# Performance work log

Hardware: AMD Instinct MI355X
Metric: run time of the kernel (lower is better)

## Reference

```python
import jax, jax.numpy as jnp
import numpy as np
import math

D_QKV = 64


def setup_inputs() -> dict:
    key = jax.random.key(0)
    ks = jax.random.split(key, 6)
    b, l, d_model, n_head, d_qkv = 2, 2048, 1024, 16, D_QKV
    return {
        "x": jax.random.normal(ks[0], (b, l, d_model), dtype=jnp.float32),
        "w_q": jax.random.normal(ks[1], (n_head, d_model, d_qkv), dtype=jnp.float32) * (2.0 / (d_model + d_qkv)) ** 0.5,
        "w_k": jax.random.normal(ks[2], (n_head, d_model, d_qkv), dtype=jnp.float32) * (2.0 / (d_model + d_qkv)) ** 0.5,
        "w_v": jax.random.normal(ks[3], (n_head, d_model, d_qkv), dtype=jnp.float32) * (2.0 / (d_model + d_qkv)) ** 0.5,
        "w_o": jax.random.normal(ks[4], (n_head, d_qkv, d_model), dtype=jnp.float32) * (2.0 / (d_model + d_qkv)) ** 0.5,
        "mask": jnp.zeros((b, 1, 1, l), dtype=bool),  # True = masked (padding)
    }


def reference(x, w_q, w_k, w_v, w_o, mask):
    # x: [b, l, m]; w_{q,k,v}: [n, m, d]; w_o: [n, d, m]; mask broadcastable to [b, n, l, l]
    q = jnp.einsum("blm,nmd->bnld", x, w_q)
    k = jnp.einsum("blm,nmd->bnld", x, w_k)
    v = jnp.einsum("blm,nmd->bnld", x, w_v)
    scores = jnp.einsum("bnld,bnkd->bnlk", q, k) / math.sqrt(D_QKV)
    scores = jnp.where(mask, jnp.float32(-1e9), scores)
    attn = jax.nn.softmax(scores, axis=-1)  # dropout is identity (p=0 / eval)
    ctx = jnp.einsum("bnlk,bnkd->bnld", attn, v)
    # per-head output projection then sum over heads: V.matmul(w_o).sum(dim=1)
    return jnp.einsum("bnld,ndm->blm", ctx, w_o)
```

## Files before the change

### kernel.cpp

```cpp
#include <hip/hip_runtime.h>
#include <stdint.h>

using bf16x8  = __attribute__((ext_vector_type(8))) short;
using f32x4   = __attribute__((ext_vector_type(4))) float;
using f32x16  = __attribute__((ext_vector_type(16))) float;
using ushort8 = __attribute__((ext_vector_type(8))) unsigned short;
using ushort4v= __attribute__((ext_vector_type(4))) unsigned short;
using uint2v  = __attribute__((ext_vector_type(2))) unsigned int;

typedef __attribute__((address_space(1))) const unsigned int* gas_ptr;
typedef __attribute__((address_space(3))) unsigned int*       las_ptr;

__device__ __forceinline__ void gload_lds16(const unsigned short* g, unsigned short* l) {
    __builtin_amdgcn_global_load_lds((gas_ptr)(const void*)g, (las_ptr)(void*)l, 16, 0, 0);
}

__device__ __forceinline__ unsigned short f2bf(float f) {
    union { float f; uint32_t u; } x; x.f = f;
    uint32_t u = x.u;
    uint32_t r = u + 0x7fffu + ((u >> 16) & 1u);
    return (unsigned short)(r >> 16);
}
__device__ __forceinline__ float bf2f(unsigned short u) {
    union { uint32_t u; float f; } x; x.u = ((uint32_t)u) << 16;
    return x.f;
}

__device__ __forceinline__ f32x4 mfma16(bf16x8 a, bf16x8 b, f32x4 c) {
    return __builtin_amdgcn_mfma_f32_16x16x32_bf16(a, b, c, 0, 0, 0);
}
__device__ __forceinline__ f32x16 mfma32(bf16x8 a, bf16x8 b, f32x16 c) {
    return __builtin_amdgcn_mfma_f32_32x32x16_bf16(a, b, c, 0, 0, 0);
}

__device__ __forceinline__ unsigned int cvtpk_bf16(float lo, float hi) {
    unsigned int r;
    asm("v_cvt_pk_bf16_f32 %0, %1, %2" : "=v"(r) : "v"(lo), "v"(hi));
    return r;
}
__device__ __forceinline__ void plswap(unsigned int& a, unsigned int& b) {
    asm("v_permlane32_swap_b32 %0, %1" : "+v"(a), "+v"(b));
}


__global__ void cast_x_kernel(const float* __restrict__ x, unsigned short* __restrict__ xb) {
    int i = blockIdx.x * 256 + threadIdx.x;
    using f32x4v = __attribute__((ext_vector_type(4))) float;
    f32x4v v = ((const f32x4v*)x)[i];
    ushort4v o;
    o[0] = f2bf(v[0]); o[1] = f2bf(v[1]); o[2] = f2bf(v[2]); o[3] = f2bf(v[3]);
    ((ushort4v*)xb)[i] = o;
}

__global__ void pack_wqkv_t(const float* __restrict__ wq, const float* __restrict__ wk,
                            const float* __restrict__ wv, unsigned short* __restrict__ wpT) {
    __shared__ float tile[64][65];
    const int mm = blockIdx.y;
    const int s = mm >> 4, hh = mm & 15;
    const float* src = ((s == 0) ? wq : (s == 1) ? wk : wv) + (size_t)hh * 1024 * 64;
    const int k0 = blockIdx.x * 64;
    const int c = threadIdx.x & 63, rg = threadIdx.x >> 6;
#pragma unroll
    for (int i = 0; i < 16; ++i) {
        int r = rg * 16 + i;
        tile[r][c] = src[(size_t)(k0 + r) * 64 + c];
    }
    __syncthreads();
    unsigned short* dst = wpT + ((size_t)s * 1024 + hh * 64) * 1024 + k0;
    const int kc = threadIdx.x & 63, dg = threadIdx.x >> 6;
#pragma unroll
    for (int i = 0; i < 16; ++i) {
        int d = dg * 16 + i;
        dst[(size_t)d * 1024 + kc] = f2bf(tile[kc][d]);
    }
}

__global__ void pack_wo_t(const float* __restrict__ wo, unsigned short* __restrict__ woT) {
    __shared__ float tile[64][65];
    const int r0 = blockIdx.y * 64;
    const int c0 = blockIdx.x * 64;
    const int c = threadIdx.x & 63, rg = threadIdx.x >> 6;
#pragma unroll
    for (int i = 0; i < 16; ++i) {
        int r = rg * 16 + i;
        tile[r][c] = wo[(size_t)(r0 + r) * 1024 + c0 + c];
    }
    __syncthreads();
    const int kc = threadIdx.x & 63, mg = threadIdx.x >> 6;
#pragma unroll
    for (int i = 0; i < 16; ++i) {
        int m = mg * 16 + i;
        woT[(size_t)(c0 + m) * 1024 + r0 + kc] = f2bf(tile[kc][m]);
    }
}

__global__ void vt_kernel(const unsigned short* __restrict__ vb, unsigned short* __restrict__ vtb) {
    __shared__ unsigned short tile[64][72];
    const int bh = blockIdx.y;
    const int l0 = blockIdx.x * 64;
    const unsigned short* src = vb + (size_t)bh * 131072;
    unsigned short* dst = vtb + (size_t)bh * 131072;
    const int c8 = threadIdx.x & 7, r2 = threadIdx.x >> 3;
#pragma unroll
    for (int it = 0; it < 2; ++it) {
        int r = r2 + it * 32;
        ushort8 v = *(const ushort8*)&src[(size_t)(l0 + r) * 64 + c8 * 8];
        *(ushort8*)&tile[r][c8 * 8] = v;
    }
    __syncthreads();
#pragma unroll
    for (int it = 0; it < 2; ++it) {
        int d = r2 + it * 32;
        ushort8 o;
#pragma unroll
        for (int j = 0; j < 8; ++j) o[j] = tile[c8 * 8 + j][d];
        *(ushort8*)&dst[(size_t)d * 2048 + l0 + c8 * 8] = o;
    }
}


template<int MODE, int BN>
__global__ __launch_bounds__(256) void gemm_bt(
    const unsigned short* __restrict__ A,
    const unsigned short* __restrict__ BT,
    float* __restrict__ Cf,
    unsigned short* __restrict__ Q,
    unsigned short* __restrict__ Kq,
    unsigned short* __restrict__ V,
    int M, int N, int K)
{
    constexpr int NF = BN / 32;
    __shared__ unsigned short As[128 * 64];
    __shared__ unsigned short Bs[BN * 64];
    const int tid  = threadIdx.x;
    const int lane = tid & 63;
    const int wave = tid >> 6;
    const int wm = wave >> 1, wn = wave & 1;
    const int l15 = lane & 15, l4 = lane >> 4;
    const int row0 = blockIdx.y * 128;
    const int col0 = blockIdx.x * BN;

    f32x4 acc[4][NF];
#pragma unroll
    for (int i = 0; i < 4; ++i)
#pragma unroll
        for (int j = 0; j < NF; ++j) acc[i][j] = (f32x4){0.f, 0.f, 0.f, 0.f};

    for (int k0 = 0; k0 < K; k0 += 64) {
        __syncthreads();
#pragma unroll
        for (int it = 0; it < 4; ++it) {
            int cb = (it * 4 + wave) * 64;
            int c  = cb + lane;
            int r  = c >> 3, c8 = c & 7;
            int sc8 = c8 ^ (r & 7);
            gload_lds16(&A[(size_t)(row0 + r) * K + k0 + sc8 * 8], &As[cb * 8]);
        }
#pragma unroll
        for (int it = 0; it < NF; ++it) {
            int cb = (it * 4 + wave) * 64;
            int c  = cb + lane;
            int r  = c >> 3, c8 = c & 7;
            int sc8 = c8 ^ (r & 7);
            gload_lds16(&BT[(size_t)(col0 + r) * K + k0 + sc8 * 8], &Bs[cb * 8]);
        }
        __syncthreads();
#pragma unroll
        for (int kk = 0; kk < 2; ++kk) {
            bf16x8 af[4], bfr[NF];
#pragma unroll
            for (int m = 0; m < 4; ++m) {
                int r   = wm * 64 + m * 16 + l15;
                int blk = (kk * 4 + l4) ^ (r & 7);
                af[m] = *(const bf16x8*)&As[r * 64 + blk * 8];
            }
#pragma unroll
            for (int n = 0; n < NF; ++n) {
                int r   = wn * (BN / 2) + n * 16 + l15;
                int blk = (kk * 4 + l4) ^ (r & 7);
                bfr[n] = *(const bf16x8*)&Bs[r * 64 + blk * 8];
            }
#pragma unroll
            for (int m = 0; m < 4; ++m)
#pragma unroll
                for (int n = 0; n < NF; ++n)
                    acc[m][n] = mfma16(af[m], bfr[n], acc[m][n]);
        }
    }

#pragma unroll
    for (int m = 0; m < 4; ++m) {
#pragma unroll
        for (int n = 0; n < NF; ++n) {
#pragma unroll
            for (int r = 0; r < 4; ++r) {
                int gr = row0 + wm * 64 + m * 16 + l4 * 4 + r;
                int gc = col0 + wn * (BN / 2) + n * 16 + l15;
                float v = acc[m][n][r];
                if (MODE == 0) {
                    int s = gc >> 10, rem = gc & 1023;
                    int hh = rem >> 6, dd = rem & 63;
                    int bb = gr >> 11, ll = gr & 2047;
                    unsigned short* dst = (s == 0) ? Q : (s == 1) ? Kq : V;
                    dst[(((size_t)bb * 16 + hh) * 2048 + ll) * 64 + dd] = f2bf(v);
                } else {
                    Cf[(size_t)gr * N + gc] = v;
                }
            }
        }
    }
}


__global__ __launch_bounds__(256, 4) void attn_kernel(
    const unsigned short* __restrict__ qb,
    const unsigned short* __restrict__ kb,
    const unsigned short* __restrict__ vtb,
    const unsigned char* __restrict__ mask,
    unsigned short* __restrict__ part0,
    unsigned short* __restrict__ part1,
    float* __restrict__ ml)
{
    const int lg = blockIdx.x;
    int u = ((lg & 7) << 7) | (lg >> 3);
    int bh = u >> 5, sub = u & 31;
    const int qt = sub >> 1, half = sub & 1;
    const int b = bh >> 4, h = bh & 15;
    const int t0 = half * 16;
    const int NT = 16;

    const int tid  = threadIdx.x;
    const int lane = tid & 63, wave = tid >> 6;
    const int l31  = lane & 31, hi = lane >> 5;

    __shared__ unsigned short smem[16384];
    __shared__ int flags[32];

    const size_t hoff = (size_t)bh * 131072;
    const unsigned short* qh  = qb  + hoff;
    const unsigned short* kh  = kb  + hoff;
    const unsigned short* vth = vtb + hoff;
    const unsigned char*  mb  = mask + (size_t)b * 2048;

    if (tid < 32) flags[tid] = 0;
    __syncthreads();
    {
        uint2v mv = *(const uint2v*)&mb[tid * 8];
        if (mv[0] | mv[1]) flags[tid >> 3] = 1;
    }

    const int qrow = qt * 128 + wave * 32 + l31;
    bf16x8 qf[4];
#pragma unroll
    for (int ki = 0; ki < 4; ++ki)
        qf[ki] = *(const bf16x8*)&qh[(size_t)qrow * 64 + ki * 16 + hi * 8];

    f32x16 accA = {0,0,0,0,0,0,0,0,0,0,0,0,0,0,0,0};
    f32x16 accB = {0,0,0,0,0,0,0,0,0,0,0,0,0,0,0,0};
    float m_r = -1e30f, l_r = 0.f;
    const float SC  = 0.18033688011112042f;
    const float THR = 44.3614195558365f;

#define STAGE(KB, VB, KV0) do {                                                          \
        _Pragma("unroll")                                                                \
        for (int it_ = 0; it_ < 2; ++it_) {                                              \
            int c_ = it_ * 256 + tid;                                                    \
            int r_ = c_ >> 3, c8_ = c_ & 7;                                              \
            int sc8_ = c8_ ^ (r_ & 7);                                                   \
            gload_lds16(&kh[(size_t)((KV0) + r_) * 64 + sc8_ * 8],                       \
                        &(KB)[(it_ * 256 + wave * 64) * 8]);                             \
            gload_lds16(&vth[(size_t)r_ * 2048 + (KV0) + sc8_ * 8],                      \
                        &(VB)[(it_ * 256 + wave * 64) * 8]);                             \
        }                                                                                \
    } while (0)

    STAGE(smem, smem + 8192, t0 * 64);

    for (int t = t0; t < t0 + NT; ++t) {
        const int kv0 = t * 64;
        unsigned short* Kb = smem + ((t - t0) & 1) * 4096;
        unsigned short* Vb = smem + 8192 + ((t - t0) & 1) * 4096;
        __syncthreads();
        if (t + 1 < t0 + NT) {
            unsigned short* Kn = smem + ((t + 1 - t0) & 1) * 4096;
            unsigned short* Vn = smem + 8192 + ((t + 1 - t0) & 1) * 4096;
            STAGE(Kn, Vn, kv0 + 64);
        }

        f32x16 s0 = {0,0,0,0,0,0,0,0,0,0,0,0,0,0,0,0};
        f32x16 s1 = {0,0,0,0,0,0,0,0,0,0,0,0,0,0,0,0};
        __builtin_amdgcn_s_setprio(1);
#pragma unroll
        for (int ki = 0; ki < 4; ++ki) {
            int c0 = ((ki * 2 + hi) ^ (l31 & 7)) * 8;
            bf16x8 a0 = *(const bf16x8*)&Kb[l31 * 64 + c0];
            bf16x8 a1 = *(const bf16x8*)&Kb[(32 + l31) * 64 + c0];
            s0 = mfma32(a0, qf[ki], s0);
            s1 = mfma32(a1, qf[ki], s1);
        }
        __builtin_amdgcn_s_setprio(0);

        if (flags[t]) {
#pragma unroll
            for (int r = 0; r < 16; ++r) {
                int keyl = (r & 3) + 8 * (r >> 2) + 4 * hi;
                if (mb[kv0 + keyl])      s0[r] = -1e30f;
                if (mb[kv0 + 32 + keyl]) s1[r] = -1e30f;
            }
        }

        float mx;
        {
            float a0 = fmaxf(fmaxf(s0[0], s0[1]),  fmaxf(s0[2],  s0[3]));
            float a1 = fmaxf(fmaxf(s0[4], s0[5]),  fmaxf(s0[6],  s0[7]));
            float a2 = fmaxf(fmaxf(s0[8], s0[9]),  fmaxf(s0[10], s0[11]));
            float a3 = fmaxf(fmaxf(s0[12], s0[13]), fmaxf(s0[14], s0[15]));
            float b0 = fmaxf(fmaxf(s1[0], s1[1]),  fmaxf(s1[2],  s1[3]));
            float b1 = fmaxf(fmaxf(s1[4], s1[5]),  fmaxf(s1[6],  s1[7]));
            float b2 = fmaxf(fmaxf(s1[8], s1[9]),  fmaxf(s1[10], s1[11]));
            float b3 = fmaxf(fmaxf(s1[12], s1[13]), fmaxf(s1[14], s1[15]));
            mx = fmaxf(fmaxf(fmaxf(a0, a1), fmaxf(a2, a3)),
                       fmaxf(fmaxf(b0, b1), fmaxf(b2, b3)));
        }
        mx = fmaxf(mx, __shfl_xor(mx, 32));
        if (__any(mx > m_r + THR)) {
            float mn  = fmaxf(m_r, mx);
            float scl = __builtin_amdgcn_exp2f((m_r - mn) * SC);
            m_r = mn;
            l_r *= scl;
#pragma unroll
            for (int i = 0; i < 16; ++i) { accA[i] *= scl; accB[i] *= scl; }
        }
        const float nmc = -m_r * SC;
#pragma unroll
        for (int i = 0; i < 16; ++i) {
            s0[i] = __builtin_amdgcn_exp2f(__builtin_fmaf(s0[i], SC, nmc));
            s1[i] = __builtin_amdgcn_exp2f(__builtin_fmaf(s1[i], SC, nmc));
        }
        float rs;
        {
            float a0 = (s0[0] + s0[1]) + (s0[2] + s0[3]);
            float a1 = (s0[4] + s0[5]) + (s0[6] + s0[7]);
            float a2 = (s0[8] + s0[9]) + (s0[10] + s0[11]);
            float a3 = (s0[12] + s0[13]) + (s0[14] + s0[15]);
            float b0 = (s1[0] + s1[1]) + (s1[2] + s1[3]);
            float b1 = (s1[4] + s1[5]) + (s1[6] + s1[7]);
            float b2 = (s1[8] + s1[9]) + (s1[10] + s1[11]);
            float b3 = (s1[12] + s1[13]) + (s1[14] + s1[15]);
            rs = ((a0 + a1) + (a2 + a3)) + ((b0 + b1) + (b2 + b3));
        }
        rs += __shfl_xor(rs, 32);
        l_r += rs;

        bf16x8 pf[4];
        {
            union { unsigned int u[4]; bf16x8 v; } f;
            unsigned int w0 = cvtpk_bf16(s0[0],  s0[1]),  w1 = cvtpk_bf16(s0[2],  s0[3]);
            unsigned int w2 = cvtpk_bf16(s0[4],  s0[5]),  w3 = cvtpk_bf16(s0[6],  s0[7]);
            unsigned int w4 = cvtpk_bf16(s0[8],  s0[9]),  w5 = cvtpk_bf16(s0[10], s0[11]);
            unsigned int w6 = cvtpk_bf16(s0[12], s0[13]), w7 = cvtpk_bf16(s0[14], s0[15]);
            plswap(w0, w2); plswap(w1, w3); plswap(w4, w6); plswap(w5, w7);
            f.u[0] = w0; f.u[1] = w1; f.u[2] = w2; f.u[3] = w3; pf[0] = f.v;
            f.u[0] = w4; f.u[1] = w5; f.u[2] = w6; f.u[3] = w7; pf[1] = f.v;
            unsigned int x0 = cvtpk_bf16(s1[0],  s1[1]),  x1 = cvtpk_bf16(s1[2],  s1[3]);
            unsigned int x2 = cvtpk_bf16(s1[4],  s1[5]),  x3 = cvtpk_bf16(s1[6],  s1[7]);
            unsigned int x4 = cvtpk_bf16(s1[8],  s1[9]),  x5 = cvtpk_bf16(s1[10], s1[11]);
            unsigned int x6 = cvtpk_bf16(s1[12], s1[13]), x7 = cvtpk_bf16(s1[14], s1[15]);
            plswap(x0, x2); plswap(x1, x3); plswap(x4, x6); plswap(x5, x7);
            f.u[0] = x0; f.u[1] = x1; f.u[2] = x2; f.u[3] = x3; pf[2] = f.v;
            f.u[0] = x4; f.u[1] = x5; f.u[2] = x6; f.u[3] = x7; pf[3] = f.v;
        }

        __builtin_amdgcn_s_setprio(1);
#pragma unroll
        for (int ks = 0; ks < 4; ++ks) {
            int c0 = ((ks * 2 + hi) ^ (l31 & 7)) * 8;
            bf16x8 vA = *(const bf16x8*)&Vb[l31 * 64 + c0];
            bf16x8 vB = *(const bf16x8*)&Vb[(32 + l31) * 64 + c0];
            accA = mfma32(vA, pf[ks], accA);
            accB = mfma32(vB, pf[ks], accB);
        }
        __builtin_amdgcn_s_setprio(0);
    }
#undef STAGE

    __syncthreads();
    const int qloc = wave * 32 + l31;
#pragma unroll
    for (int r = 0; r < 16; ++r) {
        int dA = (r & 3) + 8 * (r >> 2) + 4 * hi;
        smem[qloc * 64 + (dA ^ ((qloc & 7) * 8))]        = f2bf(accA[r]);
        smem[qloc * 64 + ((32 + dA) ^ ((qloc & 7) * 8))] = f2bf(accB[r]);
    }
    if (hi == 0) {
        size_t mrow = ((size_t)half * 32 + bh) * 2048 + qt * 128 + qloc;
        *(float2*)&ml[mrow * 2] = make_float2(m_r, l_r);
    }
    __syncthreads();
    unsigned short* pdst = half ? part1 : part0;
    const size_t prow0 = (size_t)bh * 2048 + qt * 128;
#pragma unroll
    for (int it = 0; it < 4; ++it) {
        int idx = tid + it * 256;
        int q = idx >> 3, c = idx & 7;
        ushort8 vv = *(const ushort8*)&smem[q * 64 + ((c * 8) ^ ((q & 7) * 8))];
        *(ushort8*)&pdst[(prow0 + q) * 64 + c * 8] = vv;
    }
}


__global__ void combine_kernel(const unsigned short* __restrict__ part0,
                               const unsigned short* __restrict__ part1,
                               const float* __restrict__ ml,
                               unsigned short* __restrict__ ctxb)
{
    const float SC = 0.18033688011112042f;
    int gid = blockIdx.x * 256 + threadIdx.x;
    int row = gid >> 3, c = gid & 7;
    ushort8 v0 = *(const ushort8*)&part0[(size_t)row * 64 + c * 8];
    ushort8 v1 = *(const ushort8*)&part1[(size_t)row * 64 + c * 8];
    float2 a = *(const float2*)&ml[(size_t)row * 2];
    float2 d = *(const float2*)&ml[(size_t)(65536 + row) * 2];
    float m  = fmaxf(a.x, d.x);
    float w0 = __builtin_amdgcn_exp2f((a.x - m) * SC);
    float w1 = __builtin_amdgcn_exp2f((d.x - m) * SC);
    float li = 1.0f / (a.y * w0 + d.y * w1);
    ushort8 o;
#pragma unroll
    for (int j = 0; j < 8; ++j)
        o[j] = f2bf((bf2f(v0[j]) * w0 + bf2f(v1[j]) * w1) * li);
    int bh = row >> 11, ql = row & 2047;
    int bb = bh >> 4, hh = bh & 15;
    *(ushort8*)&ctxb[((size_t)(bb * 2048 + ql)) * 1024 + hh * 64 + c * 8] = o;
}


extern "C" void kernel_launch(void* const* d_in, const int* in_sizes, int n_in,
                              void* d_out, int out_size, void* d_ws, size_t ws_size,
                              hipStream_t stream)
{
    const float* x  = (const float*)d_in[0];
    const float* wq = (const float*)d_in[1];
    const float* wk = (const float*)d_in[2];
    const float* wv = (const float*)d_in[3];
    const float* wo = (const float*)d_in[4];
    const unsigned char* mask = (const unsigned char*)d_in[5];
    float* out = (float*)d_out;

    char* ws = (char*)d_ws;
    unsigned short* xb   = (unsigned short*)(ws);
    unsigned short* wpT  = (unsigned short*)(ws + 8388608);
    unsigned short* woT  = (unsigned short*)(ws + 14680064);
    unsigned short* qb   = (unsigned short*)(ws + 16777216);
    unsigned short* kb   = (unsigned short*)(ws + 25165824);
    unsigned short* vb   = (unsigned short*)(ws + 33554432);
    unsigned short* ctxb = (unsigned short*)(ws + 41943040);
    unsigned short* vtb   = xb;
    unsigned short* part0 = (unsigned short*)d_out;
    unsigned short* part1 = (unsigned short*)d_out + 4194304;
    float*          mlb   = (float*)wpT;

    cast_x_kernel<<<4096, 256, 0, stream>>>(x, xb);
    pack_wqkv_t  <<<dim3(16, 48), 256, 0, stream>>>(wq, wk, wv, wpT);
    pack_wo_t    <<<dim3(16, 16), 256, 0, stream>>>(wo, woT);

    gemm_bt<0,128><<<dim3(24, 32), 256, 0, stream>>>(xb, wpT, nullptr, qb, kb, vb, 4096, 3072, 1024);

    vt_kernel<<<dim3(32, 32), 256, 0, stream>>>(vb, vtb);
    attn_kernel<<<1024, 256, 0, stream>>>(qb, kb, vtb, mask, part0, part1, mlb);
    combine_kernel<<<2048, 256, 0, stream>>>(part0, part1, mlb, ctxb);

    gemm_bt<1,64><<<dim3(16, 32), 256, 0, stream>>>(ctxb, woT, out, nullptr, nullptr, nullptr, 4096, 1024, 1024);
}
```

Before: 133.4 us.

## Write V transposed from QKV GEMM epilogue and compute row sums via MFMA

The QKV projection epilogue now writes V directly in transposed [d, l] layout with 4-wide vector stores, so the separate vt_kernel launch and its round trip through memory go away. The attention kernel drops the per-tile scalar row-sum reduction and cross-lane shuffle. Instead it accumulates the softmax denominator with an extra MFMA against a vector of bf16 ones. The max reduction is rewritten with three-input max patterns, and the first QK MFMA takes a zero accumulator instead of zeroing explicitly. In exchange, each PV step issues one more MFMA and the row sum is taken from bf16-rounded probabilities.

```diff
diff --git a/kernel.cpp b/kernel.cpp
--- a/kernel.cpp
+++ b/kernel.cpp
@@ -40,6 +40,9 @@
 }
 __device__ __forceinline__ void plswap(unsigned int& a, unsigned int& b) {
     asm("v_permlane32_swap_b32 %0, %1" : "+v"(a), "+v"(b));
+}
+__device__ __forceinline__ float m3(float a, float b, float c) {
+    return fmaxf(fmaxf(a, b), c);
 }
 
 
@@ -91,30 +94,6 @@
     for (int i = 0; i < 16; ++i) {
         int m = mg * 16 + i;
         woT[(size_t)(c0 + m) * 1024 + r0 + kc] = f2bf(tile[kc][m]);
-    }
-}
-
-__global__ void vt_kernel(const unsigned short* __restrict__ vb, unsigned short* __restrict__ vtb) {
-    __shared__ unsigned short tile[64][72];
-    const int bh = blockIdx.y;
-    const int l0 = blockIdx.x * 64;
-    const unsigned short* src = vb + (size_t)bh * 131072;
-    unsigned short* dst = vtb + (size_t)bh * 131072;
-    const int c8 = threadIdx.x & 7, r2 = threadIdx.x >> 3;
-#pragma unroll
-    for (int it = 0; it < 2; ++it) {
-        int r = r2 + it * 32;
-        ushort8 v = *(const ushort8*)&src[(size_t)(l0 + r) * 64 + c8 * 8];
-        *(ushort8*)&tile[r][c8 * 8] = v;
-    }
-    __syncthreads();
-#pragma unroll
-    for (int it = 0; it < 2; ++it) {
-        int d = r2 + it * 32;
-        ushort8 o;
-#pragma unroll
-        for (int j = 0; j < 8; ++j) o[j] = tile[c8 * 8 + j][d];
-        *(ushort8*)&dst[(size_t)d * 2048 + l0 + c8 * 8] = o;
     }
 }
 
@@ -190,22 +169,29 @@
 
 #pragma unroll
     for (int m = 0; m < 4; ++m) {
+        int gr0 = row0 + wm * 64 + m * 16 + l4 * 4;
 #pragma unroll
         for (int n = 0; n < NF; ++n) {
-#pragma unroll
-            for (int r = 0; r < 4; ++r) {
-                int gr = row0 + wm * 64 + m * 16 + l4 * 4 + r;
-                int gc = col0 + wn * (BN / 2) + n * 16 + l15;
-                float v = acc[m][n][r];
-                if (MODE == 0) {
-                    int s = gc >> 10, rem = gc & 1023;
-                    int hh = rem >> 6, dd = rem & 63;
-                    int bb = gr >> 11, ll = gr & 2047;
-                    unsigned short* dst = (s == 0) ? Q : (s == 1) ? Kq : V;
-                    dst[(((size_t)bb * 16 + hh) * 2048 + ll) * 64 + dd] = f2bf(v);
+            int gc = col0 + wn * (BN / 2) + n * 16 + l15;
+            if (MODE == 0) {
+                int s = gc >> 10, rem = gc & 1023;
+                int hh = rem >> 6, dd = rem & 63;
+                int bb = gr0 >> 11, ll = gr0 & 2047;
+                if (s == 2) {
+                    ushort4v o;
+#pragma unroll
+                    for (int r = 0; r < 4; ++r) o[r] = f2bf(acc[m][n][r]);
+                    *(ushort4v*)&V[(((size_t)bb * 16 + hh) * 64 + dd) * 2048 + ll] = o;
                 } else {
-                    Cf[(size_t)gr * N + gc] = v;
+                    unsigned short* dst = (s == 0) ? Q : Kq;
+#pragma unroll
+                    for (int r = 0; r < 4; ++r)
+                        dst[(((size_t)bb * 16 + hh) * 2048 + ll + r) * 64 + dd] = f2bf(acc[m][n][r]);
                 }
+            } else {
+#pragma unroll
+                for (int r = 0; r < 4; ++r)
+                    Cf[(size_t)(gr0 + r) * N + gc] = acc[m][n][r];
             }
         }
     }
@@ -225,7 +211,7 @@
     int u = ((lg & 7) << 7) | (lg >> 3);
     int bh = u >> 5, sub = u & 31;
     const int qt = sub >> 1, half = sub & 1;
-    const int b = bh >> 4, h = bh & 15;
+    const int b = bh >> 4;
     const int t0 = half * 16;
     const int NT = 16;
 
@@ -255,9 +241,15 @@
     for (int ki = 0; ki < 4; ++ki)
         qf[ki] = *(const bf16x8*)&qh[(size_t)qrow * 64 + ki * 16 + hi * 8];
 
+    const f32x16 zf = {0,0,0,0,0,0,0,0,0,0,0,0,0,0,0,0};
+    bf16x8 ones;
+#pragma unroll
+    for (int j = 0; j < 8; ++j) ones[j] = (short)0x3F80;
+
     f32x16 accA = {0,0,0,0,0,0,0,0,0,0,0,0,0,0,0,0};
     f32x16 accB = {0,0,0,0,0,0,0,0,0,0,0,0,0,0,0,0};
-    float m_r = -1e30f, l_r = 0.f;
+    f32x16 accL = {0,0,0,0,0,0,0,0,0,0,0,0,0,0,0,0};
+    float m_r = -1e30f;
     const float SC  = 0.18033688011112042f;
     const float THR = 44.3614195558365f;
 
@@ -287,11 +279,17 @@
             STAGE(Kn, Vn, kv0 + 64);
         }
 
-        f32x16 s0 = {0,0,0,0,0,0,0,0,0,0,0,0,0,0,0,0};
-        f32x16 s1 = {0,0,0,0,0,0,0,0,0,0,0,0,0,0,0,0};
+        f32x16 s0, s1;
         __builtin_amdgcn_s_setprio(1);
-#pragma unroll
-        for (int ki = 0; ki < 4; ++ki) {
+        {
+            int c0 = (hi ^ (l31 & 7)) * 8;
+            bf16x8 a0 = *(const bf16x8*)&Kb[l31 * 64 + c0];
+            bf16x8 a1 = *(const bf16x8*)&Kb[(32 + l31) * 64 + c0];
+            s0 = mfma32(a0, qf[0], zf);
+            s1 = mfma32(a1, qf[0], zf);
+        }
+#pragma unroll
+        for (int ki = 1; ki < 4; ++ki) {
             int c0 = ((ki * 2 + hi) ^ (l31 & 7)) * 8;
             bf16x8 a0 = *(const bf16x8*)&Kb[l31 * 64 + c0];
             bf16x8 a1 = *(const bf16x8*)&Kb[(32 + l31) * 64 + c0];
@@ -311,23 +309,28 @@
 
         float mx;
         {
-            float a0 = fmaxf(fmaxf(s0[0], s0[1]),  fmaxf(s0[2],  s0[3]));
-            float a1 = fmaxf(fmaxf(s0[4], s0[5]),  fmaxf(s0[6],  s0[7]));
-            float a2 = fmaxf(fmaxf(s0[8], s0[9]),  fmaxf(s0[10], s0[11]));
-            float a3 = fmaxf(fmaxf(s0[12], s0[13]), fmaxf(s0[14], s0[15]));
-            float b0 = fmaxf(fmaxf(s1[0], s1[1]),  fmaxf(s1[2],  s1[3]));
-            float b1 = fmaxf(fmaxf(s1[4], s1[5]),  fmaxf(s1[6],  s1[7]));
-            float b2 = fmaxf(fmaxf(s1[8], s1[9]),  fmaxf(s1[10], s1[11]));
-            float b3 = fmaxf(fmaxf(s1[12], s1[13]), fmaxf(s1[14], s1[15]));
-            mx = fmaxf(fmaxf(fmaxf(a0, a1), fmaxf(a2, a3)),
-                       fmaxf(fmaxf(b0, b1), fmaxf(b2, b3)));
+            float a0 = m3(s0[0],  s0[1],  s0[2]);
+            float a1 = m3(s0[3],  s0[4],  s0[5]);
+            float a2 = m3(s0[6],  s0[7],  s0[8]);
+            float a3 = m3(s0[9],  s0[10], s0[11]);
+            float a4 = m3(s0[12], s0[13], s0[14]);
+            float b0 = m3(s1[0],  s1[1],  s1[2]);
+            float b1 = m3(s1[3],  s1[4],  s1[5]);
+            float b2 = m3(s1[6],  s1[7],  s1[8]);
+            float b3 = m3(s1[9],  s1[10], s1[11]);
+            float b4 = m3(s1[12], s1[13], s1[14]);
+            float c0 = m3(a0, a1, s0[15]);
+            float c1 = m3(a2, a3, a4);
+            float c2 = m3(b0, b1, s1[15]);
+            float c3 = m3(b2, b3, b4);
+            mx = fmaxf(m3(c0, c1, c2), c3);
         }
         mx = fmaxf(mx, __shfl_xor(mx, 32));
         if (__any(mx > m_r + THR)) {
             float mn  = fmaxf(m_r, mx);
             float scl = __builtin_amdgcn_exp2f((m_r - mn) * SC);
             m_r = mn;
-            l_r *= scl;
+            accL[0] *= scl;
 #pragma unroll
             for (int i = 0; i < 16; ++i) { accA[i] *= scl; accB[i] *= scl; }
         }
@@ -337,20 +340,6 @@
             s0[i] = __builtin_amdgcn_exp2f(__builtin_fmaf(s0[i], SC, nmc));
             s1[i] = __builtin_amdgcn_exp2f(__builtin_fmaf(s1[i], SC, nmc));
         }
-        float rs;
-        {
-            float a0 = (s0[0] + s0[1]) + (s0[2] + s0[3]);
-            float a1 = (s0[4] + s0[5]) + (s0[6] + s0[7]);
-            float a2 = (s0[8] + s0[9]) + (s0[10] + s0[11]);
-            float a3 = (s0[12] + s0[13]) + (s0[14] + s0[15]);
-            float b0 = (s1[0] + s1[1]) + (s1[2] + s1[3]);
-            float b1 = (s1[4] + s1[5]) + (s1[6] + s1[7]);
-            float b2 = (s1[8] + s1[9]) + (s1[10] + s1[11]);
-            float b3 = (s1[12] + s1[13]) + (s1[14] + s1[15]);
-            rs = ((a0 + a1) + (a2 + a3)) + ((b0 + b1) + (b2 + b3));
-        }
-        rs += __shfl_xor(rs, 32);
-        l_r += rs;
 
         bf16x8 pf[4];
         {
@@ -379,6 +368,7 @@
             bf16x8 vB = *(const bf16x8*)&Vb[(32 + l31) * 64 + c0];
             accA = mfma32(vA, pf[ks], accA);
             accB = mfma32(vB, pf[ks], accB);
+            accL = mfma32(ones, pf[ks], accL);
         }
         __builtin_amdgcn_s_setprio(0);
     }
@@ -394,7 +384,7 @@
     }
     if (hi == 0) {
         size_t mrow = ((size_t)half * 32 + bh) * 2048 + qt * 128 + qloc;
-        *(float2*)&ml[mrow * 2] = make_float2(m_r, l_r);
+        *(float2*)&ml[mrow * 2] = make_float2(m_r, accL[0]);
     }
     __syncthreads();
     unsigned short* pdst = half ? part1 : part0;
@@ -453,9 +443,8 @@
     unsigned short* woT  = (unsigned short*)(ws + 14680064);
     unsigned short* qb   = (unsigned short*)(ws + 16777216);
     unsigned short* kb   = (unsigned short*)(ws + 25165824);
-    unsigned short* vb   = (unsigned short*)(ws + 33554432);
+    unsigned short* vtb  = (unsigned short*)(ws + 33554432);
     unsigned short* ctxb = (unsigned short*)(ws + 41943040);
-    unsigned short* vtb   = xb;
     unsigned short* part0 = (unsigned short*)d_out;
     unsigned short* part1 = (unsigned short*)d_out + 4194304;
     float*          mlb   = (float*)wpT;
@@ -464,9 +453,8 @@
     pack_wqkv_t  <<<dim3(16, 48), 256, 0, stream>>>(wq, wk, wv, wpT);
     pack_wo_t    <<<dim3(16, 16), 256, 0, stream>>>(wo, woT);
 
-    gemm_bt<0,128><<<dim3(24, 32), 256, 0, stream>>>(xb, wpT, nullptr, qb, kb, vb, 4096, 3072, 1024);
-
-    vt_kernel<<<dim3(32, 32), 256, 0, stream>>>(vb, vtb);
+    gemm_bt<0,128><<<dim3(24, 32), 256, 0, stream>>>(xb, wpT, nullptr, qb, kb, vtb, 4096, 3072, 1024);
+
     attn_kernel<<<1024, 256, 0, stream>>>(qb, kb, vtb, mask, part0, part1, mlb);
     combine_kernel<<<2048, 256, 0, stream>>>(part0, part1, mlb, ctxb);
 
```

Measured after the change: 128.3 us. -3.8%, faster.
